# Kernel optimization log

Measured on AMD Instinct MI355X. Metric: run time of the kernel, lower is better.

The kernel has to match this reference:

```python
import jax, jax.numpy as jnp
import numpy as np

ALPHA_1 = 0.5
ALPHA_2 = 0.9
TAU = 0.1
BIG_NUM = 1.0e9


def setup_inputs() -> dict:
    key = jax.random.key(0)
    k1, k2 = jax.random.split(key)
    B, N_SUP, N_QRY, D = 4, 512, 4096, 128
    features = jax.random.normal(k1, (B, N_SUP + N_QRY, D), dtype=jnp.float32)
    support_labels = jax.random.randint(k2, (B, N_SUP), 0, 64, dtype=jnp.int64)
    return {"features": features, "support_labels": support_labels}


def _sq_dists(x, y):
    # squared Euclidean pairwise distances: [B, N, M]
    xn = jnp.sum(x * x, axis=-1)  # [B, N]
    yn = jnp.sum(y * y, axis=-1)  # [B, M]
    xy = jnp.einsum('bnd,bmd->bnm', x, y)
    return xn[:, :, None] + yn[:, None, :] - 2.0 * xy


def reference(features, support_labels):
    n_support = support_labels.shape[1]
    support = features[:, :n_support]   # [B, S, D]
    query = features[:, n_support:]     # [B, Q, D]

    # --- re_represent_queries ---
    logits = -TAU * _sq_dists(query, query)           # [B, Q, Q]
    Q = query.shape[1]
    rng = jnp.arange(Q)
    logits = logits.at[:, rng, rng].set(-BIG_NUM)     # mask self-similarity
    attn_q = jax.nn.softmax(logits, axis=2)
    # Faithful to source: (attn[:,:,:,None] * q[:,:,None,:]).sum(2)
    # i.e. row index of q matches row index of attn; softmax axis j is contracted
    # against a broadcast copy of the same row.
    re_rep_q = jnp.einsum('bij,bid->bid', attn_q, query)
    new_query = (1.0 - ALPHA_1) * query + ALPHA_1 * re_rep_q

    # --- re_represent_supports ---
    logits_s = -TAU * _sq_dists(support, new_query)   # [B, S, Q]
    attn_s = jax.nn.softmax(logits_s, axis=2)
    re_rep_s = jnp.einsum('bsq,bqd->bsd', attn_s, new_query)
    new_support = (1.0 - ALPHA_2) * support + ALPHA_2 * re_rep_s

    return jnp.concatenate((new_support, new_query), axis=1)
```

## Files before the change

### kernel.cpp

```cpp
#include <hip/hip_runtime.h>

#define BATCH 4
#define NS 512
#define NQ 4096
#define D 128
#define NTOT (NS + NQ)

#define NCHUNK 16
#define QCHUNK (NQ / NCHUNK)
#define QT 64
#define ST 64
#define PITN 136
#define PITT 72

typedef __attribute__((ext_vector_type(8))) short bf16x8;
typedef __attribute__((ext_vector_type(4))) float f32x4;

#define L2E 1.4426950408889634f
#define SCL 0.28853900817779268f

__device__ __forceinline__ unsigned short f2bf(float f) {
    unsigned int x = __float_as_uint(f);
    return (unsigned short)((x + 0x7fffu + ((x >> 16) & 1u)) >> 16);
}

__device__ __forceinline__ unsigned int pk2(float a, float b) {
#if __has_builtin(__builtin_amdgcn_cvt_pk_bf16_f32)
    typedef __bf16 bf2 __attribute__((ext_vector_type(2)));
    bf2 r = __builtin_amdgcn_cvt_pk_bf16_f32(a, b);
    return __builtin_bit_cast(unsigned int, r);
#else
    return (unsigned)f2bf(a) | ((unsigned)f2bf(b) << 16);
#endif
}

__global__ __launch_bounds__(256) void attend_kernel(const float* __restrict__ feat,
                                                     float* __restrict__ out,
                                                     unsigned int* __restrict__ accPk,
                                                     float* __restrict__ lsumP) {
    __shared__ unsigned short qn_[QT * PITN];
    __shared__ unsigned short qt_[D * PITT];
    __shared__ unsigned short p_[ST * PITT];
    __shared__ float qns[QCHUNK];

    int chunk = blockIdx.x, stile = blockIdx.y, b = blockIdx.z;
    int s0 = stile * ST;
    int q0 = chunk * QCHUNK;
    int t = threadIdx.x;
    int w = t >> 6, ln = t & 15, quad = (t >> 4) & 3;

    const float* srow = feat + ((size_t)b * NTOT + s0 + 16 * w + ln) * D;
    bf16x8 asup[4];
    #pragma unroll
    for (int kk = 0; kk < 4; ++kk) {
        float4 lo = *(const float4*)(srow + 32 * kk + 8 * quad);
        float4 hi = *(const float4*)(srow + 32 * kk + 8 * quad + 4);
        union { bf16x8 v; unsigned int u[4]; } pk;
        pk.u[0] = pk2(lo.x, lo.y);
        pk.u[1] = pk2(lo.z, lo.w);
        pk.u[2] = pk2(hi.x, hi.y);
        pk.u[3] = pk2(hi.z, hi.w);
        asup[kk] = pk.v;
    }

    f32x4 cpv[8];
    #pragma unroll
    for (int ds = 0; ds < 8; ++ds) cpv[ds] = (f32x4){0.f, 0.f, 0.f, 0.f};
    float lpart[4] = {0.f, 0.f, 0.f, 0.f};

    int qrow = t >> 2;
    int dgrp = (t & 3) * 4;
    const float* qchunk_base = feat + ((size_t)b * NTOT + NS + q0) * D;
    float* outq = out + ((size_t)b * NTOT + NS + q0) * D;
    int copy_qt = (stile >> 1) << 6;
    int copy_ok = (qrow >> 5) == (stile & 1);

    for (int qt = 0; qt < QCHUNK; qt += QT) {
        __syncthreads();
        const float* qbase = qchunk_base + (size_t)(qt + qrow) * D;
        float nrm = 0.f;
        int docopy = (qt == copy_qt) & copy_ok;
        #pragma unroll
        for (int i = 0; i < 8; ++i) {
            int d = dgrp + 16 * i;
            float4 v = *(const float4*)(qbase + d);
            if (docopy) *(float4*)(outq + (size_t)(qt + qrow) * D + d) = v;
            nrm += v.x * v.x + v.y * v.y + v.z * v.z + v.w * v.w;
            unsigned int p01 = pk2(v.x, v.y);
            unsigned int p23 = pk2(v.z, v.w);
            *(uint2*)&qn_[qrow * PITN + d] = make_uint2(p01, p23);
            qt_[(d + 0) * PITT + qrow] = (unsigned short)p01;
            qt_[(d + 1) * PITT + qrow] = (unsigned short)(p01 >> 16);
            qt_[(d + 2) * PITT + qrow] = (unsigned short)p23;
            qt_[(d + 3) * PITT + qrow] = (unsigned short)(p23 >> 16);
        }
        nrm += __shfl_xor(nrm, 1, 64);
        nrm += __shfl_xor(nrm, 2, 64);
        if ((t & 3) == 0) qns[qt + qrow] = 0.1f * L2E * nrm;
        __syncthreads();

        f32x4 cqk[4];
        #pragma unroll
        for (int f = 0; f < 4; ++f) cqk[f] = (f32x4){0.f, 0.f, 0.f, 0.f};
        #pragma unroll
        for (int kk = 0; kk < 4; ++kk) {
            #pragma unroll
            for (int f = 0; f < 4; ++f) {
                bf16x8 bq = *(const bf16x8*)&qn_[(16 * f + ln) * PITN + 32 * kk + 8 * quad];
                cqk[f] = __builtin_amdgcn_mfma_f32_16x16x32_bf16(asup[kk], bq, cqk[f], 0, 0, 0);
            }
        }

        #pragma unroll
        for (int f = 0; f < 4; ++f) {
            float qs = qns[qt + 16 * f + ln];
            #pragma unroll
            for (int r = 0; r < 4; r += 2) {
                float e0 = exp2f(SCL * cqk[f][r]     - qs);
                float e1 = exp2f(SCL * cqk[f][r + 1] - qs);
                lpart[r] += e0;
                lpart[r + 1] += e1;
                unsigned int pe = pk2(e0, e1);
                p_[(16 * w + 4 * quad + r)     * PITT + 16 * f + ln] = (unsigned short)pe;
                p_[(16 * w + 4 * quad + r + 1) * PITT + 16 * f + ln] = (unsigned short)(pe >> 16);
            }
        }

        #pragma unroll
        for (int kk = 0; kk < 2; ++kk) {
            bf16x8 ap = *(const bf16x8*)&p_[(16 * w + ln) * PITT + 32 * kk + 8 * quad];
            #pragma unroll
            for (int ds = 0; ds < 8; ++ds) {
                bf16x8 bv = *(const bf16x8*)&qt_[(16 * ds + ln) * PITT + 32 * kk + 8 * quad];
                cpv[ds] = __builtin_amdgcn_mfma_f32_16x16x32_bf16(ap, bv, cpv[ds], 0, 0, 0);
            }
        }
    }

    int base = (chunk * BATCH + b) * NS + s0;
    #pragma unroll
    for (int r = 0; r < 4; ++r) {
        float v = lpart[r];
        v += __shfl_xor(v, 1, 64);
        v += __shfl_xor(v, 2, 64);
        v += __shfl_xor(v, 4, 64);
        v += __shfl_xor(v, 8, 64);
        if (ln == 0) lsumP[base + 16 * w + 4 * quad + r] = v;
    }
    #pragma unroll
    for (int ds = 0; ds < 4; ++ds)
        #pragma unroll
        for (int r = 0; r < 4; ++r)
            accPk[(size_t)(base + 16 * w + 4 * quad + r) * 64 + 16 * ds + ln] =
                pk2(cpv[ds][r], cpv[ds + 4][r]);
}

__global__ __launch_bounds__(256) void epi_kernel(const float* __restrict__ feat,
                                                  const unsigned int* __restrict__ accPk,
                                                  const float* __restrict__ lsumP,
                                                  float* __restrict__ out) {
    int wave = threadIdx.x >> 6;
    int lane = threadIdx.x & 63;
    int row = blockIdx.x * 4 + wave;
    int b = row >> 9;
    int s = row & (NS - 1);

    float l = 0.f, a0 = 0.f, a1 = 0.f;
    #pragma unroll 4
    for (int c = 0; c < NCHUNK; ++c) {
        int base = (c * BATCH + b) * NS + s;
        l += lsumP[base];
        unsigned int pw = accPk[(size_t)base * 64 + lane];
        a0 += __uint_as_float(pw << 16);
        a1 += __uint_as_float(pw & 0xffff0000u);
    }
    float inv = 0.9f / l;
    size_t fo = ((size_t)b * NTOT + s) * D;
    float s0v = feat[fo + lane];
    float s1v = feat[fo + lane + 64];
    out[fo + lane]      = 0.1f * s0v + a0 * inv;
    out[fo + lane + 64] = 0.1f * s1v + a1 * inv;
}

extern "C" void kernel_launch(void* const* d_in, const int* in_sizes, int n_in,
                              void* d_out, int out_size, void* d_ws, size_t ws_size,
                              hipStream_t stream) {
    const float* feat = (const float*)d_in[0];
    float* out = (float*)d_out;
    unsigned int* accPk = (unsigned int*)d_ws;
    float* lsumP = (float*)(accPk + (size_t)NCHUNK * BATCH * NS * 64);
    (void)in_sizes; (void)n_in; (void)out_size; (void)ws_size;

    attend_kernel<<<dim3(NCHUNK, NS / ST, BATCH), 256, 0, stream>>>(feat, out, accPk, lsumP);
    epi_kernel<<<BATCH * NS / 4, 256, 0, stream>>>(feat, accPk, lsumP, out);
}
```

Baseline: 83.24 us.

## Prefetch next query tile into registers and XOR-swizzle transposed LDS tile

The query-tile staging is restructured so each thread loads 4 rows by 8 columns. The next tile's global loads are issued right after the barrier, so they overlap with the MFMA and exp work. The transposed tile qt_ drops its padded pitch for an XOR-swizzled 64-wide layout, which allows packed 4-element uint2 stores in place of scalar 16-bit stores while avoiding bank conflicts on reads. Holding the prefetch in registers raises register pressure, and the extra final prefetch wraps around to a redundant load.

New measurement: 81.83 us (median of 2 runs). Within noise of the previous version (-1.7%).

```diff
diff --git a/kernel.cpp b/kernel.cpp
--- a/kernel.cpp
+++ b/kernel.cpp
@@ -11,7 +11,7 @@
 #define QT 64
 #define ST 64
 #define PITN 136
-#define PITT 72
+#define PITP 72
 
 typedef __attribute__((ext_vector_type(8))) short bf16x8;
 typedef __attribute__((ext_vector_type(4))) float f32x4;
@@ -34,20 +34,41 @@
 #endif
 }
 
+__device__ __forceinline__ int qtIdx(int row, int col) {
+    return ((row << 6) | col) ^ ((((row >> 3) ^ row) & 7) << 3);
+}
+
 __global__ __launch_bounds__(256) void attend_kernel(const float* __restrict__ feat,
                                                      float* __restrict__ out,
                                                      unsigned int* __restrict__ accPk,
                                                      float* __restrict__ lsumP) {
-    __shared__ unsigned short qn_[QT * PITN];
-    __shared__ unsigned short qt_[D * PITT];
-    __shared__ unsigned short p_[ST * PITT];
-    __shared__ float qns[QCHUNK];
+    __shared__ __align__(16) unsigned short qn_[QT * PITN];
+    __shared__ __align__(16) unsigned short qt_[D * 64];
+    __shared__ __align__(16) unsigned short p_[ST * PITP];
+    __shared__ __align__(16) float qns[QCHUNK];
 
     int chunk = blockIdx.x, stile = blockIdx.y, b = blockIdx.z;
     int s0 = stile * ST;
     int q0 = chunk * QCHUNK;
     int t = threadIdx.x;
     int w = t >> 6, ln = t & 15, quad = (t >> 4) & 3;
+
+    int qgrp = t >> 4;
+    int qr0  = qgrp << 2;
+    int dl   = t & 15;
+    int d0   = dl << 3;
+
+    const float* qchunk_base = feat + ((size_t)b * NTOT + NS + q0) * D;
+    float* outq = out + ((size_t)b * NTOT + NS + q0) * D;
+
+    float4 f0a, f0b, f1a, f1b, f2a, f2b, f3a, f3b;
+    {
+        const float* p = qchunk_base + (size_t)qr0 * D + d0;
+        f0a = *(const float4*)p;           f0b = *(const float4*)(p + 4);
+        f1a = *(const float4*)(p + D);     f1b = *(const float4*)(p + D + 4);
+        f2a = *(const float4*)(p + 2 * D); f2b = *(const float4*)(p + 2 * D + 4);
+        f3a = *(const float4*)(p + 3 * D); f3b = *(const float4*)(p + 3 * D + 4);
+    }
 
     const float* srow = feat + ((size_t)b * NTOT + s0 + 16 * w + ln) * D;
     bf16x8 asup[4];
@@ -68,36 +89,60 @@
     for (int ds = 0; ds < 8; ++ds) cpv[ds] = (f32x4){0.f, 0.f, 0.f, 0.f};
     float lpart[4] = {0.f, 0.f, 0.f, 0.f};
 
-    int qrow = t >> 2;
-    int dgrp = (t & 3) * 4;
-    const float* qchunk_base = feat + ((size_t)b * NTOT + NS + q0) * D;
-    float* outq = out + ((size_t)b * NTOT + NS + q0) * D;
     int copy_qt = (stile >> 1) << 6;
-    int copy_ok = (qrow >> 5) == (stile & 1);
+    int copy_ok = (qr0 >> 5) == (stile & 1);
 
     for (int qt = 0; qt < QCHUNK; qt += QT) {
         __syncthreads();
-        const float* qbase = qchunk_base + (size_t)(qt + qrow) * D;
-        float nrm = 0.f;
+
         int docopy = (qt == copy_qt) & copy_ok;
-        #pragma unroll
-        for (int i = 0; i < 8; ++i) {
-            int d = dgrp + 16 * i;
-            float4 v = *(const float4*)(qbase + d);
-            if (docopy) *(float4*)(outq + (size_t)(qt + qrow) * D + d) = v;
-            nrm += v.x * v.x + v.y * v.y + v.z * v.z + v.w * v.w;
-            unsigned int p01 = pk2(v.x, v.y);
-            unsigned int p23 = pk2(v.z, v.w);
-            *(uint2*)&qn_[qrow * PITN + d] = make_uint2(p01, p23);
-            qt_[(d + 0) * PITT + qrow] = (unsigned short)p01;
-            qt_[(d + 1) * PITT + qrow] = (unsigned short)(p01 >> 16);
-            qt_[(d + 2) * PITT + qrow] = (unsigned short)p23;
-            qt_[(d + 3) * PITT + qrow] = (unsigned short)(p23 >> 16);
-        }
-        nrm += __shfl_xor(nrm, 1, 64);
-        nrm += __shfl_xor(nrm, 2, 64);
-        if ((t & 3) == 0) qns[qt + qrow] = 0.1f * L2E * nrm;
+        float nr0, nr1, nr2, nr3;
+        #define ROWW(r, va, vb) { \
+            union { bf16x8 v; unsigned int u[4]; } pk; \
+            pk.u[0] = pk2(va.x, va.y); pk.u[1] = pk2(va.z, va.w); \
+            pk.u[2] = pk2(vb.x, vb.y); pk.u[3] = pk2(vb.z, vb.w); \
+            *(bf16x8*)&qn_[(qr0 + r) * PITN + d0] = pk.v; \
+            nr##r = va.x*va.x + va.y*va.y + va.z*va.z + va.w*va.w \
+                  + vb.x*vb.x + vb.y*vb.y + vb.z*vb.z + vb.w*vb.w; \
+            if (docopy) { \
+                float* op = outq + (size_t)(qt + qr0 + r) * D + d0; \
+                *(float4*)op = va; *(float4*)(op + 4) = vb; \
+            } }
+        ROWW(0, f0a, f0b)
+        ROWW(1, f1a, f1b)
+        ROWW(2, f2a, f2b)
+        ROWW(3, f3a, f3b)
+        #undef ROWW
+
+        #define QTW(j, e0, e1, e2, e3) \
+            *(uint2*)&qt_[qtIdx(d0 + j, qr0)] = make_uint2(pk2(e0, e1), pk2(e2, e3));
+        QTW(0, f0a.x, f1a.x, f2a.x, f3a.x)
+        QTW(1, f0a.y, f1a.y, f2a.y, f3a.y)
+        QTW(2, f0a.z, f1a.z, f2a.z, f3a.z)
+        QTW(3, f0a.w, f1a.w, f2a.w, f3a.w)
+        QTW(4, f0b.x, f1b.x, f2b.x, f3b.x)
+        QTW(5, f0b.y, f1b.y, f2b.y, f3b.y)
+        QTW(6, f0b.z, f1b.z, f2b.z, f3b.z)
+        QTW(7, f0b.w, f1b.w, f2b.w, f3b.w)
+        #undef QTW
+
+        #define RED4(x) x += __shfl_xor(x, 1, 64); x += __shfl_xor(x, 2, 64); \
+                        x += __shfl_xor(x, 4, 64); x += __shfl_xor(x, 8, 64);
+        RED4(nr0) RED4(nr1) RED4(nr2) RED4(nr3)
+        #undef RED4
+        if (dl == 0)
+            *(float4*)&qns[qt + qr0] = make_float4(0.1f * L2E * nr0, 0.1f * L2E * nr1,
+                                                   0.1f * L2E * nr2, 0.1f * L2E * nr3);
         __syncthreads();
+
+        {
+            int qtn = (qt + QT) & (QCHUNK - 1);
+            const float* p = qchunk_base + (size_t)(qtn + qr0) * D + d0;
+            f0a = *(const float4*)p;           f0b = *(const float4*)(p + 4);
+            f1a = *(const float4*)(p + D);     f1b = *(const float4*)(p + D + 4);
+            f2a = *(const float4*)(p + 2 * D); f2b = *(const float4*)(p + 2 * D + 4);
+            f3a = *(const float4*)(p + 3 * D); f3b = *(const float4*)(p + 3 * D + 4);
+        }
 
         f32x4 cqk[4];
         #pragma unroll
@@ -121,17 +166,17 @@
                 lpart[r] += e0;
                 lpart[r + 1] += e1;
                 unsigned int pe = pk2(e0, e1);
-                p_[(16 * w + 4 * quad + r)     * PITT + 16 * f + ln] = (unsigned short)pe;
-                p_[(16 * w + 4 * quad + r + 1) * PITT + 16 * f + ln] = (unsigned short)(pe >> 16);
+                p_[(16 * w + 4 * quad + r)     * PITP + 16 * f + ln] = (unsigned short)pe;
+                p_[(16 * w + 4 * quad + r + 1) * PITP + 16 * f + ln] = (unsigned short)(pe >> 16);
             }
         }
 
         #pragma unroll
         for (int kk = 0; kk < 2; ++kk) {
-            bf16x8 ap = *(const bf16x8*)&p_[(16 * w + ln) * PITT + 32 * kk + 8 * quad];
+            bf16x8 ap = *(const bf16x8*)&p_[(16 * w + ln) * PITP + 32 * kk + 8 * quad];
             #pragma unroll
             for (int ds = 0; ds < 8; ++ds) {
-                bf16x8 bv = *(const bf16x8*)&qt_[(16 * ds + ln) * PITT + 32 * kk + 8 * quad];
+                bf16x8 bv = *(const bf16x8*)&qt_[qtIdx(16 * ds + ln, 32 * kk + 8 * quad)];
                 cpv[ds] = __builtin_amdgcn_mfma_f32_16x16x32_bf16(ap, bv, cpv[ds], 0, 0, 0);
             }
         }
```
